# Kernel tuning notes

Measured on AMD Instinct MI355X. Metric: run time of the kernel, lower is better.

## Reference

```python
import jax, jax.numpy as jnp
import numpy as np
import math

N_EMBD = 1024
N_HEAD = 16
HEAD_DIM = N_EMBD // N_HEAD
SEQ = 2048
BATCH = 2
EPS = 1e-5


def _gelu_tanh(x):
    c = math.sqrt(2.0 / math.pi)
    return 0.5 * x * (1.0 + jnp.tanh(c * (x + 0.044715 * x ** 3)))


def _layernorm(x, w, b):
    mean = jnp.mean(x, axis=-1, keepdims=True)
    var = jnp.mean(jnp.square(x - mean), axis=-1, keepdims=True)  # unbiased=False
    return (x - mean) / jnp.sqrt(var + EPS) * w + b


def setup_inputs() -> dict:
    key = jax.random.key(0)
    ks = jax.random.split(key, 8)
    D = N_EMBD
    s = 0.02
    return {
        "x": jax.random.normal(ks[0], (BATCH, SEQ, D), jnp.float32),
        "ln1_w": jnp.ones((D,), jnp.float32),
        "ln1_b": jnp.zeros((D,), jnp.float32),
        "w_qkv": jax.random.normal(ks[1], (D, 3 * D), jnp.float32) * s,
        "b_qkv": jnp.zeros((3 * D,), jnp.float32),
        "w_attn_proj": jax.random.normal(ks[2], (D, D), jnp.float32) * s,
        "b_attn_proj": jnp.zeros((D,), jnp.float32),
        "ln2_w": jnp.ones((D,), jnp.float32),
        "ln2_b": jnp.zeros((D,), jnp.float32),
        "w_fc": jax.random.normal(ks[3], (D, 4 * D), jnp.float32) * s,
        "b_fc": jnp.zeros((4 * D,), jnp.float32),
        "w_proj": jax.random.normal(ks[4], (4 * D, D), jnp.float32) * s,
        "b_proj": jnp.zeros((D,), jnp.float32),
    }


def reference(x, ln1_w, ln1_b, w_qkv, b_qkv, w_attn_proj, b_attn_proj,
              ln2_w, ln2_b, w_fc, b_fc, w_proj, b_proj):
    bs, T, D = x.shape
    # --- attention branch (pre-LN) ---
    h = _layernorm(x, ln1_w, ln1_b)
    qkv = h @ w_qkv + b_qkv                      # [B,T,3D]
    q, k, v = jnp.split(qkv, 3, axis=-1)
    q = q.reshape(bs, T, N_HEAD, HEAD_DIM).transpose(0, 2, 1, 3)  # [B,H,T,d]
    k = k.reshape(bs, T, N_HEAD, HEAD_DIM).transpose(0, 2, 1, 3)
    v = v.reshape(bs, T, N_HEAD, HEAD_DIM).transpose(0, 2, 1, 3)
    scores = jnp.einsum("bhqd,bhkd->bhqk", q, k) * (1.0 / math.sqrt(HEAD_DIM))
    causal = jnp.tril(jnp.ones((T, T), bool))
    scores = jnp.where(causal[None, None], scores, -jnp.inf)
    att = jax.nn.softmax(scores, axis=-1)
    ctx = jnp.einsum("bhqk,bhkd->bhqd", att, v)
    ctx = ctx.transpose(0, 2, 1, 3).reshape(bs, T, D)
    attn_out = ctx @ w_attn_proj + b_attn_proj
    x = x + attn_out
    # --- MLP branch (pre-LN) ---
    h = _layernorm(x, ln2_w, ln2_b)
    h = _gelu_tanh(h @ w_fc + b_fc)
    h = h @ w_proj + b_proj
    return x + h
```

## Files before the change

### kernel.cpp

```cpp
#include <hip/hip_runtime.h>

typedef unsigned short u16;
typedef __attribute__((ext_vector_type(8))) __bf16 bf16x8;
typedef __attribute__((ext_vector_type(8))) unsigned short ushort8;
typedef __attribute__((ext_vector_type(4))) float f32x4;

#define MFMA16(a, b, c) __builtin_amdgcn_mfma_f32_16x16x32_bf16((a), (b), (c), 0, 0, 0)

__device__ __forceinline__ u16 f2bf(float f) {
  union { __bf16 h; u16 u; } cv;
  cv.h = (__bf16)f;
  return cv.u;
}

__device__ __forceinline__ void async16(const u16* g, u16* l) {
  __builtin_amdgcn_global_load_lds(
      (const __attribute__((address_space(1))) void*)g,
      (__attribute__((address_space(3))) void*)l, 16, 0, 0);
}

__global__ __launch_bounds__(256)
void transpose_bf16(const float* __restrict__ W, u16* __restrict__ Wt, int K, int N) {
  __shared__ float t[32][33];
  const int n0 = blockIdx.x * 32, k0 = blockIdx.y * 32;
  const int tx = threadIdx.x, ty = threadIdx.y;
  #pragma unroll
  for (int i = 0; i < 32; i += 8)
    t[ty + i][tx] = W[(size_t)(k0 + ty + i) * N + n0 + tx];
  __syncthreads();
  #pragma unroll
  for (int i = 0; i < 32; i += 8)
    Wt[(size_t)(n0 + ty + i) * K + k0 + tx] = f2bf(t[tx][ty + i]);
}

__global__ __launch_bounds__(256)
void transpose_v(const u16* __restrict__ v, u16* __restrict__ vt) {
  __shared__ u16 t[64][72];
  const int bh = blockIdx.y, t0 = blockIdx.x * 64;
  const int tid = threadIdx.x;
  #pragma unroll
  for (int s = 0; s < 2; ++s) {
    const int idx = tid + s * 256;
    const int row = idx >> 3, ch = idx & 7;
    ushort8 d = *(const ushort8*)(v + ((size_t)bh * 2048 + t0 + row) * 64 + ch * 8);
    #pragma unroll
    for (int e = 0; e < 8; ++e) t[ch * 8 + e][row] = d[e];
  }
  __syncthreads();
  #pragma unroll
  for (int s = 0; s < 2; ++s) {
    const int idx = tid + s * 256;
    const int drow = idx >> 3, ch = idx & 7;
    ushort8 o = *(const ushort8*)(&t[drow][ch * 8]);
    *(ushort8*)(vt + ((size_t)bh * 64 + drow) * 2048 + t0 + ch * 8) = o;
  }
}

__global__ __launch_bounds__(256)
void ln_bf16(const float* __restrict__ X, const float* __restrict__ w,
             const float* __restrict__ bia, u16* __restrict__ out) {
  const int row = blockIdx.x, tid = threadIdx.x;
  const float4 v = ((const float4*)(X + (size_t)row * 1024))[tid];
  float s = v.x + v.y + v.z + v.w;
  float s2 = v.x * v.x + v.y * v.y + v.z * v.z + v.w * v.w;
  #pragma unroll
  for (int o = 32; o > 0; o >>= 1) { s += __shfl_down(s, o); s2 += __shfl_down(s2, o); }
  __shared__ float red[8];
  const int wv = tid >> 6, lane = tid & 63;
  if (lane == 0) { red[wv] = s; red[4 + wv] = s2; }
  __syncthreads();
  s = red[0] + red[1] + red[2] + red[3];
  s2 = red[4] + red[5] + red[6] + red[7];
  const float mean = s * (1.f / 1024.f);
  const float var = s2 * (1.f / 1024.f) - mean * mean;
  const float rstd = rsqrtf(var + 1e-5f);
  const float4 wv4 = ((const float4*)w)[tid];
  const float4 bv4 = ((const float4*)bia)[tid];
  ushort4 o;
  o.x = f2bf((v.x - mean) * rstd * wv4.x + bv4.x);
  o.y = f2bf((v.y - mean) * rstd * wv4.y + bv4.y);
  o.z = f2bf((v.z - mean) * rstd * wv4.z + bv4.z);
  o.w = f2bf((v.w - mean) * rstd * wv4.w + bv4.w);
  ((ushort4*)(out + (size_t)row * 1024))[tid] = o;
}

template <int MODE>
__global__ __launch_bounds__(256)
void gemm_bt(const u16* __restrict__ A, const u16* __restrict__ Bt,
             const float* __restrict__ bias, const float* __restrict__ resid,
             float* __restrict__ outF, u16* __restrict__ outB,
             u16* __restrict__ qo, u16* __restrict__ ko, u16* __restrict__ vo,
             int M, int N, int K, int kSlice) {
  __shared__ u16 As[128 * 64];
  __shared__ u16 Bs[128 * 64];
  const int tid = threadIdx.x;
  const int lane = tid & 63, wv = tid >> 6;
  const int l16 = lane & 15, quad = lane >> 4;
  const int wr = wv >> 1, wc = wv & 1;
  const int m0 = blockIdx.y * 128, n0 = blockIdx.x * 128;
  const int kBegin = blockIdx.z * kSlice, kEnd = kBegin + kSlice;
  const int srow = lane >> 3;
  const int sch = (lane & 7) ^ srow;

  f32x4 acc[4][4];
  const f32x4 fz = {0.f, 0.f, 0.f, 0.f};
  #pragma unroll
  for (int i = 0; i < 4; ++i)
    #pragma unroll
    for (int j = 0; j < 4; ++j) acc[i][j] = fz;

  for (int k0 = kBegin; k0 < kEnd; k0 += 64) {
    __syncthreads();
    #pragma unroll
    for (int s = 0; s < 4; ++s) {
      const int R = wv * 32 + s * 8;
      async16(A + (size_t)(m0 + R + srow) * K + k0 + sch * 8, As + R * 64);
      async16(Bt + (size_t)(n0 + R + srow) * K + k0 + sch * 8, Bs + R * 64);
    }
    __builtin_amdgcn_s_waitcnt(0xF70);
    __syncthreads();
    #pragma unroll
    for (int h = 0; h < 2; ++h) {
      bf16x8 af[4], bfr[4];
      #pragma unroll
      for (int i = 0; i < 4; ++i) {
        const int row = wr * 64 + i * 16 + l16;
        af[i] = *(const bf16x8*)(As + row * 64 + (((h * 4 + quad) ^ (l16 & 7)) * 8));
      }
      #pragma unroll
      for (int j = 0; j < 4; ++j) {
        const int row = wc * 64 + j * 16 + l16;
        bfr[j] = *(const bf16x8*)(Bs + row * 64 + (((h * 4 + quad) ^ (l16 & 7)) * 8));
      }
      #pragma unroll
      for (int i = 0; i < 4; ++i)
        #pragma unroll
        for (int j = 0; j < 4; ++j)
          acc[i][j] = MFMA16(af[i], bfr[j], acc[i][j]);
    }
  }

  #pragma unroll
  for (int i = 0; i < 4; ++i) {
    #pragma unroll
    for (int j = 0; j < 4; ++j) {
      const int col = n0 + wc * 64 + j * 16 + l16;
      #pragma unroll
      for (int r = 0; r < 4; ++r) {
        const int row = m0 + wr * 64 + i * 16 + quad * 4 + r;
        outF[(size_t)blockIdx.z * M * N + (size_t)row * N + col] = acc[i][j][r];
      }
    }
  }
}

template <int MODE>
__global__ __launch_bounds__(512, 2)
void gemm256(const u16* __restrict__ A, const u16* __restrict__ Bt,
             const float* __restrict__ bias, u16* __restrict__ outB,
             u16* __restrict__ qo, u16* __restrict__ ko, u16* __restrict__ vo,
             int M, int N, int K) {
  __shared__ u16 As[2][256 * 64];
  __shared__ u16 Bs[2][256 * 64];
  const int tid = threadIdx.x;
  const int lane = tid & 63, wv = tid >> 6;
  const int l16 = lane & 15, quad = lane >> 4;
  const int wr = wv >> 2, wc = wv & 3;
  const int nwg = gridDim.x, cpx = nwg >> 3;
  const int bid = (int)blockIdx.x;
  const int swz = (bid & 7) * cpx + (bid >> 3);
  const int nbx = N >> 8;
  const int m0 = (swz / nbx) * 256, n0 = (swz % nbx) * 256;
  const int sRow = lane >> 3;
  const int sCh = (lane & 7) ^ (sRow & 7);

  f32x4 acc[8][4];
  const f32x4 fz = {0.f, 0.f, 0.f, 0.f};
  #pragma unroll
  for (int i = 0; i < 8; ++i)
    #pragma unroll
    for (int j = 0; j < 4; ++j) acc[i][j] = fz;

  auto stageA = [&](int kt, int p) {
    const u16* g = A + (size_t)(m0 + wv * 8 + sRow) * K + kt * 64 + sCh * 8;
    u16* l = &As[p][(wv * 8) * 64];
    #pragma unroll
    for (int i = 0; i < 4; ++i)
      async16(g + (size_t)(i * 64) * K, l + i * 64 * 64);
  };
  auto stageB = [&](int kt, int p) {
    const u16* g = Bt + (size_t)(n0 + wv * 8 + sRow) * K + kt * 64 + sCh * 8;
    u16* l = &Bs[p][(wv * 8) * 64];
    #pragma unroll
    for (int i = 0; i < 4; ++i)
      async16(g + (size_t)(i * 64) * K, l + i * 64 * 64);
  };
  auto ldfrag = [&](const u16* base, int row, int sel) {
    return *(const bf16x8*)(base + row * 64 + ((sel ^ (row & 7)) * 8));
  };

  const int nt = K >> 6;
  stageA(0, 0);
  stageB(0, 0);
  __builtin_amdgcn_s_waitcnt(0xF70);
  __syncthreads();

  for (int kt = 0; kt < nt; ++kt) {
    const int p = kt & 1;
    const u16* Ap = As[p];
    const u16* Bp = Bs[p];
    const bool more = (kt + 1 < nt);
    bf16x8 a[4], b0[4], b1[4];

    if (more) stageA(kt + 1, p ^ 1);
    #pragma unroll
    for (int i = 0; i < 4; ++i) a[i] = ldfrag(Ap, wr * 128 + i * 16 + l16, quad);
    #pragma unroll
    for (int j = 0; j < 4; ++j) b0[j] = ldfrag(Bp, wc * 64 + j * 16 + l16, quad);
    __builtin_amdgcn_s_setprio(1);
    #pragma unroll
    for (int i = 0; i < 4; ++i)
      #pragma unroll
      for (int j = 0; j < 4; ++j) acc[i][j] = MFMA16(a[i], b0[j], acc[i][j]);
    __builtin_amdgcn_s_setprio(0);
    __builtin_amdgcn_s_barrier();

    if (more) stageB(kt + 1, p ^ 1);
    #pragma unroll
    for (int i = 0; i < 4; ++i) a[i] = ldfrag(Ap, wr * 128 + (4 + i) * 16 + l16, quad);
    __builtin_amdgcn_s_setprio(1);
    #pragma unroll
    for (int i = 0; i < 4; ++i)
      #pragma unroll
      for (int j = 0; j < 4; ++j) acc[4 + i][j] = MFMA16(a[i], b0[j], acc[4 + i][j]);
    __builtin_amdgcn_s_setprio(0);
    __builtin_amdgcn_s_barrier();

    #pragma unroll
    for (int i = 0; i < 4; ++i) a[i] = ldfrag(Ap, wr * 128 + i * 16 + l16, 4 + quad);
    #pragma unroll
    for (int j = 0; j < 4; ++j) b1[j] = ldfrag(Bp, wc * 64 + j * 16 + l16, 4 + quad);
    __builtin_amdgcn_s_setprio(1);
    #pragma unroll
    for (int i = 0; i < 4; ++i)
      #pragma unroll
      for (int j = 0; j < 4; ++j) acc[i][j] = MFMA16(a[i], b1[j], acc[i][j]);
    __builtin_amdgcn_s_setprio(0);
    __builtin_amdgcn_s_barrier();

    #pragma unroll
    for (int i = 0; i < 4; ++i) a[i] = ldfrag(Ap, wr * 128 + (4 + i) * 16 + l16, 4 + quad);
    __builtin_amdgcn_s_setprio(1);
    #pragma unroll
    for (int i = 0; i < 4; ++i)
      #pragma unroll
      for (int j = 0; j < 4; ++j) acc[4 + i][j] = MFMA16(a[i], b1[j], acc[4 + i][j]);
    __builtin_amdgcn_s_setprio(0);
    if (more) {
      __builtin_amdgcn_s_waitcnt(0xF70);
      __builtin_amdgcn_s_barrier();
      __builtin_amdgcn_sched_barrier(0);
    }
  }

  #pragma unroll
  for (int i = 0; i < 8; ++i) {
    #pragma unroll
    for (int j = 0; j < 4; ++j) {
      const int col = n0 + wc * 64 + j * 16 + l16;
      const float bc = bias[col];
      #pragma unroll
      for (int r = 0; r < 4; ++r) {
        const int row = m0 + wr * 128 + i * 16 + quad * 4 + r;
        float v = acc[i][j][r] + bc;
        if (MODE == 0) {
          const int which = col >> 10, cc = col & 1023, hh = cc >> 6, dd = cc & 63;
          const int bb = row >> 11, t = row & 2047;
          const u16 bv = f2bf(v);
          const size_t o = ((size_t)(bb * 16 + hh) * 2048 + t) * 64 + dd;
          if (which == 0)
            qo[o] = bv;
          else if (which == 1)
            ko[o] = bv;
          else
            vo[o] = bv;
        } else {
          const float x3 = v * v * v;
          const float u = 0.7978845608028654f * (v + 0.044715f * x3);
          const float e = __expf(2.f * u);
          const float th = 1.f - 2.f / (e + 1.f);
          outB[(size_t)row * N + col] = f2bf(0.5f * v * (1.f + th));
        }
      }
    }
  }
}

__global__ __launch_bounds__(256)
void reduce2(const float* __restrict__ P, const float* __restrict__ resid,
             const float* __restrict__ bias, float* __restrict__ out, int MN, int N) {
  const int idx4 = blockIdx.x * 256 + threadIdx.x;
  const size_t s = (size_t)MN >> 2;
  const float4 a = ((const float4*)P)[idx4];
  const float4 b = ((const float4*)P)[idx4 + s];
  const float4 r = ((const float4*)resid)[idx4];
  const float4 bb = ((const float4*)bias)[idx4 & (N / 4 - 1)];
  float4 o;
  o.x = r.x + a.x + b.x + bb.x;
  o.y = r.y + a.y + b.y + bb.y;
  o.z = r.z + a.z + b.z + bb.z;
  o.w = r.w + a.w + b.w + bb.w;
  ((float4*)out)[idx4] = o;
}

__global__ __launch_bounds__(256)
void reduce2_ln(const float* __restrict__ P, const float* __restrict__ resid,
                const float* __restrict__ bias, const float* __restrict__ lw,
                const float* __restrict__ lb, float* __restrict__ out,
                u16* __restrict__ h2, int MN) {
  const int row = blockIdx.x, tid = threadIdx.x;
  const int idx4 = row * 256 + tid;
  const size_t s4 = (size_t)MN >> 2;
  const float4 a = ((const float4*)P)[idx4];
  const float4 b = ((const float4*)P)[idx4 + s4];
  const float4 r = ((const float4*)resid)[idx4];
  const float4 bb = ((const float4*)bias)[tid];
  float4 o;
  o.x = r.x + a.x + b.x + bb.x;
  o.y = r.y + a.y + b.y + bb.y;
  o.z = r.z + a.z + b.z + bb.z;
  o.w = r.w + a.w + b.w + bb.w;
  ((float4*)out)[idx4] = o;
  float s = o.x + o.y + o.z + o.w;
  float s2 = o.x * o.x + o.y * o.y + o.z * o.z + o.w * o.w;
  #pragma unroll
  for (int of = 32; of > 0; of >>= 1) { s += __shfl_down(s, of); s2 += __shfl_down(s2, of); }
  __shared__ float red[8];
  const int wv = tid >> 6, lane = tid & 63;
  if (lane == 0) { red[wv] = s; red[4 + wv] = s2; }
  __syncthreads();
  s = red[0] + red[1] + red[2] + red[3];
  s2 = red[4] + red[5] + red[6] + red[7];
  const float mean = s * (1.f / 1024.f);
  const float var = s2 * (1.f / 1024.f) - mean * mean;
  const float rstd = rsqrtf(var + 1e-5f);
  const float4 wv4 = ((const float4*)lw)[tid];
  const float4 bv4 = ((const float4*)lb)[tid];
  ushort4 ob;
  ob.x = f2bf((o.x - mean) * rstd * wv4.x + bv4.x);
  ob.y = f2bf((o.y - mean) * rstd * wv4.y + bv4.y);
  ob.z = f2bf((o.z - mean) * rstd * wv4.z + bv4.z);
  ob.w = f2bf((o.w - mean) * rstd * wv4.w + bv4.w);
  ((ushort4*)(h2 + (size_t)row * 1024))[tid] = ob;
}

typedef union { bf16x8 v; unsigned d[4]; } PFU;

__global__ __launch_bounds__(512)
void attn(const u16* __restrict__ Q, const u16* __restrict__ Kg,
          const u16* __restrict__ Vt, u16* __restrict__ ctx) {
  __shared__ u16 Ks[2][128 * 64];
  __shared__ u16 Vs[64 * 128];
  const int pair = blockIdx.x;
  const int qt0 = pair, qt1 = 15 - pair;
  const int bh = blockIdx.y;
  const int b = bh >> 4, h = bh & 15;
  const int tid = threadIdx.x;
  const int lane = tid & 63, wv = tid >> 6;
  const int l16 = lane & 15, quad = lane >> 4;
  const int rb = wv * 16;
  const float S2 = 0.18033688011112042f;
  const u16* Qb = Q + (size_t)bh * 2048 * 64;
  const u16* Kb = Kg + (size_t)bh * 2048 * 64;
  const u16* Vb = Vt + (size_t)bh * 64 * 2048;

  bf16x8 qf[2][2];
  #pragma unroll
  for (int t = 0; t < 2; ++t)
    #pragma unroll
    for (int c = 0; c < 2; ++c)
      qf[t][c] = *(const bf16x8*)(Qb + (size_t)((t ? qt1 : qt0) * 128 + rb + l16) * 64 +
                                  c * 32 + quad * 8);

  f32x4 octx[2][4];
  const f32x4 fz = {0.f, 0.f, 0.f, 0.f};
  #pragma unroll
  for (int t = 0; t < 2; ++t)
    #pragma unroll
    for (int jd = 0; jd < 4; ++jd) octx[t][jd] = fz;
  float mi[2] = {-1e30f, -1e30f};
  float li[2] = {0.f, 0.f};

  const int kRow = lane >> 3, kCh = (lane & 7) ^ ((lane >> 3) & 7);
  const int vRow = lane >> 4;
  auto stageK = [&](int kt, int buf) {
    #pragma unroll
    for (int s = 0; s < 2; ++s) {
      const int R = wv * 16 + s * 8;
      async16(Kb + (size_t)(kt * 128 + R + kRow) * 64 + kCh * 8, &Ks[buf][R * 64]);
    }
  };
  auto stageV = [&](int kt) {
    #pragma unroll
    for (int s = 0; s < 2; ++s) {
      const int D = wv * 8 + s * 4;
      const int dd = D + vRow;
      const int sch = (lane & 15) ^ (dd & 15);
      async16(Vb + (size_t)dd * 2048 + kt * 128 + sch * 8, &Vs[D * 128]);
    }
  };

  const int ps0 = l16 + 16 * (2 * (quad & 1) + (quad >> 1));
  const int ps1 = ps0 ^ 16;
  const bool qlo = (quad & 1) == 0;
  const bool qh2 = (quad >> 1) == 0;

  auto qkt = [&](const u16* KsC, bf16x8* qv, f32x4* sa) {
    __builtin_amdgcn_s_setprio(1);
    #pragma unroll
    for (int j = 0; j < 8; ++j) {
      const int key7 = l16 & 7;
      bf16x8 kf0 = *(const bf16x8*)(KsC + (16 * j + l16) * 64 + ((quad ^ key7) * 8));
      bf16x8 kf1 = *(const bf16x8*)(KsC + (16 * j + l16) * 64 + (((4 + quad) ^ key7) * 8));
      sa[j] = MFMA16(kf1, qv[1], MFMA16(kf0, qv[0], fz));
    }
    __builtin_amdgcn_s_setprio(0);
  };

  auto smx = [&](f32x4* sa, int t, int kt, int qt, PFU* pf) {
    if (kt == qt) {
      const int rg = rb + l16;
      #pragma unroll
      for (int j = 0; j < 8; ++j)
        #pragma unroll
        for (int r = 0; r < 4; ++r)
          if (j * 16 + quad * 4 + r > rg) sa[j][r] = -1e30f;
    }
    float mj[8];
    #pragma unroll
    for (int j = 0; j < 8; ++j)
      mj[j] = fmaxf(fmaxf(sa[j][0], sa[j][1]), fmaxf(sa[j][2], sa[j][3]));
    float mx = fmaxf(fmaxf(fmaxf(mj[0], mj[1]), fmaxf(mj[2], mj[3])),
                     fmaxf(fmaxf(mj[4], mj[5]), fmaxf(mj[6], mj[7])));
    mx = fmaxf(mx, __shfl_xor(mx, 16));
    mx = fmaxf(mx, __shfl_xor(mx, 32));
    mx *= S2;
    const bool skip = (__all(mx - mi[t] <= 8.f) != 0);
    float mn = mi[t];
    float al = 1.f;
    if (!skip) {
      mn = fmaxf(mi[t], mx);
      al = __builtin_amdgcn_exp2f(mi[t] - mn);
      mi[t] = mn;
    }
    float r0 = 0.f, r1 = 0.f, r2 = 0.f, r3 = 0.f;
    unsigned w01[8], w23[8];
    #pragma unroll
    for (int j = 0; j < 8; ++j) {
      const float p0 = __builtin_amdgcn_exp2f(sa[j][0] * S2 - mn);
      const float p1 = __builtin_amdgcn_exp2f(sa[j][1] * S2 - mn);
      const float p2 = __builtin_amdgcn_exp2f(sa[j][2] * S2 - mn);
      const float p3 = __builtin_amdgcn_exp2f(sa[j][3] * S2 - mn);
      r0 += p0; r1 += p1; r2 += p2; r3 += p3;
      w01[j] = (unsigned)f2bf(p0) | ((unsigned)f2bf(p1) << 16);
      w23[j] = (unsigned)f2bf(p2) | ((unsigned)f2bf(p3) << 16);
    }
    float rs = (r0 + r1) + (r2 + r3);
    rs += __shfl_xor(rs, 16);
    rs += __shfl_xor(rs, 32);
    if (skip) {
      li[t] += rs;
    } else {
      li[t] = li[t] * al + rs;
      #pragma unroll
      for (int r = 0; r < 4; ++r) {
        const float alr = __shfl(al, quad * 4 + r);
        #pragma unroll
        for (int jd = 0; jd < 4; ++jd) octx[t][jd][r] *= alr;
      }
    }
    #pragma unroll
    for (int c = 0; c < 4; ++c) {
      const unsigned a0 = qlo ? w01[2 * c] : w01[2 * c + 1];
      const unsigned a1 = qlo ? w01[2 * c + 1] : w01[2 * c];
      const unsigned b0 = qlo ? w23[2 * c] : w23[2 * c + 1];
      const unsigned b1 = qlo ? w23[2 * c + 1] : w23[2 * c];
      const unsigned r00 = (unsigned)__shfl((int)a0, ps0);
      const unsigned r01 = (unsigned)__shfl((int)a1, ps1);
      const unsigned r10 = (unsigned)__shfl((int)b0, ps0);
      const unsigned r11 = (unsigned)__shfl((int)b1, ps1);
      pf[c].d[0] = qh2 ? r00 : r01;
      pf[c].d[2] = qh2 ? r01 : r00;
      pf[c].d[1] = qh2 ? r10 : r11;
      pf[c].d[3] = qh2 ? r11 : r10;
    }
  };

  auto pv = [&](PFU* pf, f32x4* oc) {
    __builtin_amdgcn_s_setprio(1);
    #pragma unroll
    for (int c = 0; c < 4; ++c) {
      #pragma unroll
      for (int jd = 0; jd < 4; ++jd) {
        const int dd = jd * 16 + l16;
        bf16x8 vf = *(const bf16x8*)(Vs + dd * 128 + (((c * 4 + quad) ^ (dd & 15)) * 8));
        oc[jd] = MFMA16(pf[c].v, vf, oc[jd]);
      }
    }
    __builtin_amdgcn_s_setprio(0);
  };

  stageK(0, 0);
  __builtin_amdgcn_s_waitcnt(0xF70);
  __syncthreads();

  for (int kt = 0; kt <= qt1; ++kt) {
    const int cur = kt & 1;
    stageV(kt);
    if (kt < qt1) stageK(kt + 1, cur ^ 1);
    const bool both = (kt <= qt0);
    const u16* KsC = Ks[cur];

    PFU pf0[4], pf1[4];
    {
      f32x4 sa[8];
      if (both) {
        qkt(KsC, qf[0], sa);
        smx(sa, 0, kt, qt0, pf0);
      }
      qkt(KsC, qf[1], sa);
      smx(sa, 1, kt, qt1, pf1);
    }

    __builtin_amdgcn_s_waitcnt(0xF70);
    __syncthreads();

    if (both) pv(pf0, octx[0]);
    pv(pf1, octx[1]);
    __syncthreads();
  }

  #pragma unroll
  for (int t = 0; t < 2; ++t) {
    const int qt = t ? qt1 : qt0;
    #pragma unroll
    for (int r = 0; r < 4; ++r) {
      const float lr = __builtin_amdgcn_rcpf(__shfl(li[t], quad * 4 + r));
      const int rowg = qt * 128 + rb + quad * 4 + r;
      #pragma unroll
      for (int jd = 0; jd < 4; ++jd) {
        const int col = h * 64 + jd * 16 + l16;
        ctx[((size_t)b * 2048 + rowg) * 1024 + col] = f2bf(octx[t][jd][r] * lr);
      }
    }
  }
}

extern "C" void kernel_launch(void* const* d_in, const int* in_sizes, int n_in,
                              void* d_out, int out_size, void* d_ws, size_t ws_size,
                              hipStream_t stream) {
  (void)in_sizes; (void)n_in; (void)out_size; (void)ws_size;
  const float* x      = (const float*)d_in[0];
  const float* ln1_w  = (const float*)d_in[1];
  const float* ln1_b  = (const float*)d_in[2];
  const float* w_qkv  = (const float*)d_in[3];
  const float* b_qkv  = (const float*)d_in[4];
  const float* w_attn = (const float*)d_in[5];
  const float* b_attn = (const float*)d_in[6];
  const float* ln2_w  = (const float*)d_in[7];
  const float* ln2_b  = (const float*)d_in[8];
  const float* w_fc   = (const float*)d_in[9];
  const float* b_fc   = (const float*)d_in[10];
  const float* w_proj = (const float*)d_in[11];
  const float* b_proj = (const float*)d_in[12];
  float* out = (float*)d_out;

  char* ws = (char*)d_ws;
  size_t off = 0;
  auto alloc = [&](size_t n) {
    char* p = ws + off;
    off += (n + 255) & ~(size_t)255;
    return p;
  };
  u16* h1     = (u16*)alloc(4096ull * 1024 * 2);
  u16* wqkvT  = (u16*)alloc(3072ull * 1024 * 2);
  u16* wattnT = (u16*)alloc(1024ull * 1024 * 2);
  u16* wfcT   = (u16*)alloc(4096ull * 1024 * 2);
  u16* wprojT = (u16*)alloc(1024ull * 4096 * 2);
  u16* q      = (u16*)alloc(4096ull * 1024 * 2);
  u16* k      = (u16*)alloc(4096ull * 1024 * 2);
  u16* vT     = (u16*)alloc(4096ull * 1024 * 2);
  u16* ctxb   = (u16*)alloc(4096ull * 1024 * 2);
  float* out1 = (float*)alloc(4096ull * 1024 * 4);
  u16* h2     = (u16*)alloc(4096ull * 1024 * 2);
  u16* fco    = (u16*)alloc(4096ull * 4096 * 2);

  u16* vtmp = ctxb;
  float* apP = (float*)fco;
  float* projP = (float*)q;

  const dim3 tb(32, 8);
  transpose_bf16<<<dim3(3072 / 32, 1024 / 32), tb, 0, stream>>>(w_qkv, wqkvT, 1024, 3072);
  transpose_bf16<<<dim3(1024 / 32, 1024 / 32), tb, 0, stream>>>(w_attn, wattnT, 1024, 1024);
  transpose_bf16<<<dim3(4096 / 32, 1024 / 32), tb, 0, stream>>>(w_fc, wfcT, 1024, 4096);
  transpose_bf16<<<dim3(1024 / 32, 4096 / 32), tb, 0, stream>>>(w_proj, wprojT, 4096, 1024);

  ln_bf16<<<4096, 256, 0, stream>>>(x, ln1_w, ln1_b, h1);

  gemm256<0><<<dim3(192), 512, 0, stream>>>(h1, wqkvT, b_qkv, nullptr, q, k, vtmp,
                                            4096, 3072, 1024);

  transpose_v<<<dim3(32, 32), 256, 0, stream>>>(vtmp, vT);

  attn<<<dim3(8, 32), 512, 0, stream>>>(q, k, vT, ctxb);

  gemm_bt<4><<<dim3(8, 32, 2), 256, 0, stream>>>(ctxb, wattnT, b_attn, nullptr, apP, nullptr,
                                                 nullptr, nullptr, nullptr, 4096, 1024, 1024, 512);
  reduce2_ln<<<4096, 256, 0, stream>>>(apP, x, b_attn, ln2_w, ln2_b, out1, h2, 4096 * 1024);

  gemm256<2><<<dim3(256), 512, 0, stream>>>(h2, wfcT, b_fc, fco, nullptr, nullptr, nullptr,
                                            4096, 4096, 1024);

  gemm_bt<4><<<dim3(8, 32, 2), 256, 0, stream>>>(fco, wprojT, b_proj, nullptr, projP, nullptr,
                                                 nullptr, nullptr, nullptr, 4096, 1024, 4096, 2048);

  reduce2<<<4096, 256, 0, stream>>>(projP, out1, b_proj, out, 4096 * 1024, 1024);
}
```

Baseline: 359.6 us.

## Deepen gemm256 pipeline to four stages with BK=32 and fewer barriers

Restructures the 256x256 GEMM main loop from a double-buffered BK=64 scheme with four intra-iteration barriers into a 4-slot ring buffer with BK=32, prefetching three tiles ahead and using one barrier per iteration. The LDS swizzle changes to match the 32-wide rows, and the waitcnt thresholds are graded by how many loads are still outstanding. The goal is to hide global-load latency better and cut synchronisation overhead. The cost is twice as many loop iterations, each with less MFMA work per barrier, and removing the occupancy hint of 2 from the launch bounds may change register allocation.

Result: no change. 363.4 us (+1.1%).

```diff
diff --git a/kernel.cpp b/kernel.cpp
--- a/kernel.cpp
+++ b/kernel.cpp
@@ -155,13 +155,13 @@
 }
 
 template <int MODE>
-__global__ __launch_bounds__(512, 2)
+__global__ __launch_bounds__(512)
 void gemm256(const u16* __restrict__ A, const u16* __restrict__ Bt,
              const float* __restrict__ bias, u16* __restrict__ outB,
              u16* __restrict__ qo, u16* __restrict__ ko, u16* __restrict__ vo,
              int M, int N, int K) {
-  __shared__ u16 As[2][256 * 64];
-  __shared__ u16 Bs[2][256 * 64];
+  __shared__ u16 As[4][256 * 32];
+  __shared__ u16 Bs[4][256 * 32];
   const int tid = threadIdx.x;
   const int lane = tid & 63, wv = tid >> 6;
   const int l16 = lane & 15, quad = lane >> 4;
@@ -171,8 +171,8 @@
   const int swz = (bid & 7) * cpx + (bid >> 3);
   const int nbx = N >> 8;
   const int m0 = (swz / nbx) * 256, n0 = (swz % nbx) * 256;
-  const int sRow = lane >> 3;
-  const int sCh = (lane & 7) ^ (sRow & 7);
+  const int sR = lane >> 2;
+  const int sc = lane & 3;
 
   f32x4 acc[8][4];
   const f32x4 fz = {0.f, 0.f, 0.f, 0.f};
@@ -181,83 +181,52 @@
     #pragma unroll
     for (int j = 0; j < 4; ++j) acc[i][j] = fz;
 
-  auto stageA = [&](int kt, int p) {
-    const u16* g = A + (size_t)(m0 + wv * 8 + sRow) * K + kt * 64 + sCh * 8;
-    u16* l = &As[p][(wv * 8) * 64];
-    #pragma unroll
-    for (int i = 0; i < 4; ++i)
-      async16(g + (size_t)(i * 64) * K, l + i * 64 * 64);
-  };
-  auto stageB = [&](int kt, int p) {
-    const u16* g = Bt + (size_t)(n0 + wv * 8 + sRow) * K + kt * 64 + sCh * 8;
-    u16* l = &Bs[p][(wv * 8) * 64];
-    #pragma unroll
-    for (int i = 0; i < 4; ++i)
-      async16(g + (size_t)(i * 64) * K, l + i * 64 * 64);
-  };
-  auto ldfrag = [&](const u16* base, int row, int sel) {
-    return *(const bf16x8*)(base + row * 64 + ((sel ^ (row & 7)) * 8));
-  };
-
-  const int nt = K >> 6;
-  stageA(0, 0);
-  stageB(0, 0);
-  __builtin_amdgcn_s_waitcnt(0xF70);
-  __syncthreads();
+  auto stage = [&](int kt) {
+    const int p = kt & 3;
+    #pragma unroll
+    for (int i = 0; i < 2; ++i) {
+      const int r = i * 128 + wv * 16 + sR;
+      const int ch = sc ^ ((r >> 1) & 3);
+      async16(A + (size_t)(m0 + r) * K + kt * 32 + ch * 8,
+              &As[p][(i * 128 + wv * 16) * 32]);
+      async16(Bt + (size_t)(n0 + r) * K + kt * 32 + ch * 8,
+              &Bs[p][(i * 128 + wv * 16) * 32]);
+    }
+  };
+  auto ldf = [&](const u16* base, int r) {
+    return *(const bf16x8*)(base + r * 32 + ((quad ^ ((r >> 1) & 3)) * 8));
+  };
+
+  const int nt = K >> 5;
+  stage(0);
+  stage(1);
+  stage(2);
+  __builtin_amdgcn_s_waitcnt(0xF78);
+  __builtin_amdgcn_s_barrier();
+  __builtin_amdgcn_sched_barrier(0);
 
   for (int kt = 0; kt < nt; ++kt) {
-    const int p = kt & 1;
-    const u16* Ap = As[p];
-    const u16* Bp = Bs[p];
-    const bool more = (kt + 1 < nt);
-    bf16x8 a[4], b0[4], b1[4];
-
-    if (more) stageA(kt + 1, p ^ 1);
-    #pragma unroll
-    for (int i = 0; i < 4; ++i) a[i] = ldfrag(Ap, wr * 128 + i * 16 + l16, quad);
-    #pragma unroll
-    for (int j = 0; j < 4; ++j) b0[j] = ldfrag(Bp, wc * 64 + j * 16 + l16, quad);
+    if (kt + 3 < nt) stage(kt + 3);
+    const u16* Ap = As[kt & 3];
+    const u16* Bp = Bs[kt & 3];
+    bf16x8 b[4];
+    #pragma unroll
+    for (int j = 0; j < 4; ++j) b[j] = ldf(Bp, wc * 64 + j * 16 + l16);
     __builtin_amdgcn_s_setprio(1);
     #pragma unroll
-    for (int i = 0; i < 4; ++i)
-      #pragma unroll
-      for (int j = 0; j < 4; ++j) acc[i][j] = MFMA16(a[i], b0[j], acc[i][j]);
+    for (int i = 0; i < 8; ++i) {
+      bf16x8 a = ldf(Ap, wr * 128 + i * 16 + l16);
+      #pragma unroll
+      for (int j = 0; j < 4; ++j) acc[i][j] = MFMA16(a, b[j], acc[i][j]);
+    }
     __builtin_amdgcn_s_setprio(0);
-    __builtin_amdgcn_s_barrier();
-
-    if (more) stageB(kt + 1, p ^ 1);
-    #pragma unroll
-    for (int i = 0; i < 4; ++i) a[i] = ldfrag(Ap, wr * 128 + (4 + i) * 16 + l16, quad);
-    __builtin_amdgcn_s_setprio(1);
-    #pragma unroll
-    for (int i = 0; i < 4; ++i)
-      #pragma unroll
-      for (int j = 0; j < 4; ++j) acc[4 + i][j] = MFMA16(a[i], b0[j], acc[4 + i][j]);
-    __builtin_amdgcn_s_setprio(0);
-    __builtin_amdgcn_s_barrier();
-
-    #pragma unroll
-    for (int i = 0; i < 4; ++i) a[i] = ldfrag(Ap, wr * 128 + i * 16 + l16, 4 + quad);
-    #pragma unroll
-    for (int j = 0; j < 4; ++j) b1[j] = ldfrag(Bp, wc * 64 + j * 16 + l16, 4 + quad);
-    __builtin_amdgcn_s_setprio(1);
-    #pragma unroll
-    for (int i = 0; i < 4; ++i)
-      #pragma unroll
-      for (int j = 0; j < 4; ++j) acc[i][j] = MFMA16(a[i], b1[j], acc[i][j]);
-    __builtin_amdgcn_s_setprio(0);
-    __builtin_amdgcn_s_barrier();
-
-    #pragma unroll
-    for (int i = 0; i < 4; ++i) a[i] = ldfrag(Ap, wr * 128 + (4 + i) * 16 + l16, 4 + quad);
-    __builtin_amdgcn_s_setprio(1);
-    #pragma unroll
-    for (int i = 0; i < 4; ++i)
-      #pragma unroll
-      for (int j = 0; j < 4; ++j) acc[4 + i][j] = MFMA16(a[i], b1[j], acc[4 + i][j]);
-    __builtin_amdgcn_s_setprio(0);
-    if (more) {
+    if (kt + 3 < nt)
+      __builtin_amdgcn_s_waitcnt(0xF78);
+    else if (kt + 2 < nt)
+      __builtin_amdgcn_s_waitcnt(0xF74);
+    else if (kt + 1 < nt)
       __builtin_amdgcn_s_waitcnt(0xF70);
+    if (kt + 1 < nt) {
       __builtin_amdgcn_s_barrier();
       __builtin_amdgcn_sched_barrier(0);
     }
```
